# Kernel optimization log

Hardware: AMD Instinct MI355X
Metric: run time of the kernel (lower is better)

The kernel has to match this reference:

```python
import jax, jax.numpy as jnp
import numpy as np

B, N, DIM = 2, 2048, 1024
HEADS, DIM_HEAD = 16, 64
SOFTCAP = 50.0
ROPE_THETA = 10000.0


def setup_inputs() -> dict:
    key = jax.random.key(0)
    k1, k2, k3 = jax.random.split(key, 3)
    x = jax.random.normal(k1, (B, N, DIM), jnp.float32)
    # structured modality positions: (type, offset, length), non-overlapping, in-bounds
    mods = np.zeros((B, 4, 3), np.int64)
    base_offsets = [200, 700, 1200, 1700]
    for b in range(B):
        for m, o in enumerate(base_offsets):
            mods[b, m] = (0, o + b * 16, 256)
    modalities = jnp.asarray(mods)
    gamma = jnp.zeros((DIM,), jnp.float32)           # RMSNorm gamma (init zeros, used as gamma+1)
    w_qkv = jax.random.normal(k2, (DIM, 3 * HEADS * DIM_HEAD), jnp.float32) * 0.02
    w_out = jax.random.normal(k3, (HEADS * DIM_HEAD, DIM), jnp.float32) * 0.02
    return {"x": x, "modalities": modalities, "gamma": gamma, "w_qkv": w_qkv, "w_out": w_out}


def _rotate_half(x):
    # interleaved-pair rotation, matching rotary-embedding-torch default
    x1, x2 = x[..., 0::2], x[..., 1::2]
    return jnp.stack((-x2, x1), axis=-1).reshape(x.shape)


def reference(x, modalities, gamma, w_qkv, w_out):
    b, n, d = x.shape
    h, dh = HEADS, DIM_HEAD
    seq = jnp.arange(n)
    off = modalities[..., 1]      # [b, m]
    length = modalities[..., 2]   # [b, m]

    # --- modality-aware rotary positions (span interior shrunk by offset [1, -1]) ---
    in_span = (seq[None, None, :] >= (off + 1)[:, :, None]) & (seq[None, None, :] < (off + length)[:, :, None])
    is_any_modality = in_span.any(axis=1)                                   # [b, n]
    pos = (seq[None, :] - jnp.cumsum(is_any_modality.astype(jnp.int32), axis=-1)).astype(jnp.float32)

    # --- RMSNorm: l2norm(x) * sqrt(d) * (gamma + 1) ---
    norm = jnp.maximum(jnp.sqrt(jnp.sum(x * x, axis=-1, keepdims=True)), 1e-12)
    xn = x / norm * jnp.sqrt(jnp.float32(d)) * (gamma + 1.0)

    # --- qkv projection, split heads -> [b, h, n, dh] ---
    qkv = (xn @ w_qkv).reshape(b, n, 3, h, dh)
    q, k, v = jnp.moveaxis(qkv, 2, 0)        # each [b, n, h, dh]
    q = jnp.transpose(q, (0, 2, 1, 3))
    k = jnp.transpose(k, (0, 2, 1, 3))
    v = jnp.transpose(v, (0, 2, 1, 3))

    # --- rotary embedding with modality-aware positions ---
    inv_freq = ROPE_THETA ** (-jnp.arange(0, dh, 2, dtype=jnp.float32) / dh)  # [dh/2]
    ang = pos[:, None, :, None] * inv_freq                                    # [b, 1, n, dh/2]
    ang = jnp.repeat(ang, 2, axis=-1)                                         # [b, 1, n, dh]
    cos, sin = jnp.cos(ang), jnp.sin(ang)
    q = q * cos + _rotate_half(q) * sin
    k = k * cos + _rotate_half(k) * sin

    # --- transfusion attention mask: causal OR per-modality bidirectional span ---
    causal_mask = seq[:, None] >= seq[None, :]                                 # [n, n]
    q_ge = seq[None, None, :] >= off[:, :, None]                               # [b, m, n]
    kv_lt = seq[None, None, :] < (off + length)[:, :, None]                    # [b, m, n]
    mod_mask = (q_ge[:, :, :, None] & kv_lt[:, :, None, :]).any(axis=1)        # [b, n, n]
    mask = causal_mask[None] | mod_mask                                        # [b, n, n]

    # --- attention with softclamp(50) ---
    scale = dh ** -0.5
    sim = jnp.einsum('bhid,bhjd->bhij', q, k) * scale
    sim = jnp.tanh(sim / SOFTCAP) * SOFTCAP
    sim = jnp.where(mask[:, None], sim, jnp.finfo(sim.dtype).min)
    attn = jax.nn.softmax(sim, axis=-1)
    out = jnp.einsum('bhij,bhjd->bhid', attn, v)                               # [b, h, n, dh]
    out = jnp.transpose(out, (0, 2, 1, 3)).reshape(b, n, h * dh)
    return out @ w_out
```

## Files before the change

### kernel.cpp

```cpp
#include <hip/hip_runtime.h>
#include <hip/hip_bf16.h>
#include <stdint.h>

#define B_ 2
#define N_ 2048
#define H_ 16
#define DIM_ 1024
#define NH3 3072
#define ROWS (B_*N_)
#define BHN (B_*H_*N_)

typedef __attribute__((ext_vector_type(8))) short bf16x8;
typedef __attribute__((ext_vector_type(4))) float f32x4;
typedef unsigned short u16;

__device__ __forceinline__ u16 f2bf(float f){
  union { float f; uint32_t u; } v; v.f = f;
  return (u16)((v.u + 0x7fffu + ((v.u >> 16) & 1u)) >> 16);
}

#if __has_builtin(__builtin_amdgcn_exp2f)
#define EXP2F(x) __builtin_amdgcn_exp2f(x)
#else
#define EXP2F(x) __expf((x) * 0.6931471805599453f)
#endif
#if __has_builtin(__builtin_amdgcn_rcpf)
#define RCPF(x) __builtin_amdgcn_rcpf(x)
#else
#define RCPF(x) (1.0f / (x))
#endif

#define GLL16(g, l) __builtin_amdgcn_global_load_lds( \
    (const __attribute__((address_space(1))) void*)(g), \
    (__attribute__((address_space(3))) void*)(l), 16, 0, 0)

__global__ __launch_bounds__(256) void k_prep(
    const float* __restrict__ x, const float* __restrict__ gamma,
    const float* __restrict__ wqkv, const float* __restrict__ wout,
    const int* __restrict__ mods,
    u16* __restrict__ xn, u16* __restrict__ wqkvT, u16* __restrict__ woutT,
    float* __restrict__ cosT, float* __restrict__ sinT)
{
  __shared__ float tile[32][33];
  const int bx = blockIdx.x;
  const int tid = threadIdx.x;
  if (bx < 4096){
    const int row = bx;
    const float4 xv = ((const float4*)(x + (size_t)row*DIM_))[tid];
    float ss = xv.x*xv.x + xv.y*xv.y + xv.z*xv.z + xv.w*xv.w;
#pragma unroll
    for (int d = 1; d < 64; d <<= 1) ss += __shfl_xor(ss, d);
    if ((tid & 63) == 0) tile[1][tid >> 6] = ss;
    __syncthreads();
    float tot = tile[1][0] + tile[1][1] + tile[1][2] + tile[1][3];
    float scl = 32.0f / fmaxf(sqrtf(tot), 1e-12f);
    const float4 gv = ((const float4*)gamma)[tid];
    ushort4 o;
    o.x = f2bf(xv.x * scl * (gv.x + 1.0f));
    o.y = f2bf(xv.y * scl * (gv.y + 1.0f));
    o.z = f2bf(xv.z * scl * (gv.z + 1.0f));
    o.w = f2bf(xv.w * scl * (gv.w + 1.0f));
    ((ushort4*)(xn + (size_t)row*DIM_))[tid] = o;
  } else if (bx < 8192){
    const int t = bx - 4096;
    const int bxx = t & 127, by = t >> 7;
    const float* src; u16* dst; int C, bc;
    if (bxx < 96){ src = wqkv; dst = wqkvT; C = NH3;  bc = bxx*32; }
    else         { src = wout; dst = woutT; C = DIM_; bc = (bxx-96)*32; }
    const int R = DIM_;
    const int tx = tid & 31, ty = tid >> 5;
    const int br = by * 32;
#pragma unroll
    for (int i = 0; i < 32; i += 8)
      tile[ty + i][tx] = src[(size_t)(br + ty + i)*C + bc + tx];
    __syncthreads();
#pragma unroll
    for (int i = 0; i < 32; i += 8)
      dst[(size_t)(bc + ty + i)*R + br + tx] = f2bf(tile[tx][ty + i]);
  } else {
    const int t = (bx - 8192)*256 + tid;
    const int f = t & 31, bn = t >> 5;
    const int b = bn >> 11, n = bn & (N_-1);
    int cum = 0;
#pragma unroll
    for (int m = 0; m < 4; ++m){
      const int off = mods[(b*4 + m)*3 + 1];
      const int len = mods[(b*4 + m)*3 + 2];
      cum += min(max(n - off, 0), len - 1);
    }
    const float pos = (float)(n - cum);
    const float inv = powf(10000.0f, -(float)(2*f) / 64.0f);
    float s, c;
    sincosf(pos * inv, &s, &c);
    cosT[t] = c; sinT[t] = s;
  }
}

template<int MODE, int BM>
__global__ __launch_bounds__(256) void k_gemm(
    const u16* __restrict__ A, const u16* __restrict__ Bt,
    int K, int Nc,
    float* __restrict__ outf,
    const float* __restrict__ cosT, const float* __restrict__ sinT,
    u16* __restrict__ qo, u16* __restrict__ ko, u16* __restrict__ vt)
{
  constexpr int MR = BM/32;
  constexpr int RA = BM/8;
  constexpr int CNT = (RA + 16)/4;
  __shared__ u16 lA[BM*64];
  __shared__ u16 lB[128*64];
  const int tid = threadIdx.x;
  const int wid = tid >> 6, lane = tid & 63;
  const int nx = gridDim.x;
  const int orig = blockIdx.y * nx + blockIdx.x;
  const int qq = (nx * gridDim.y) >> 3;
  const int wgid = (orig & 7) * qq + (orig >> 3);
  const int m0 = (wgid % nx) * BM, n0 = (wgid / nx) * 128;
  const int wm = wid >> 1, wn = wid & 1;
  const int srow = lane >> 3, sch = lane & 7;
  const int r16 = lane & 15, g4 = lane >> 4;
  f32x4 acc[MR][4] = {};
  const int ksteps = K >> 6;
  for (int kt = 0; kt < ksteps; ++kt){
    const int kb = kt*64;
    const int gch = sch ^ srow;
#pragma unroll
    for (int i = 0; i < CNT; ++i){
      const int reg = wid*CNT + i;
      if (reg < RA){
        const int row = reg*8 + srow;
        GLL16(A + (size_t)(m0 + row)*K + kb + gch*8, &lA[reg*512]);
      } else {
        const int r2 = reg - RA;
        const int row = r2*8 + srow;
        GLL16(Bt + (size_t)(n0 + row)*K + kb + gch*8, &lB[r2*512]);
      }
    }
    __syncthreads();
#pragma unroll
    for (int t = 0; t < 2; ++t){
      bf16x8 af[MR], bfr[4];
#pragma unroll
      for (int m = 0; m < MR; ++m){
        int row = wm*(BM/2) + m*16 + r16;
        int ch = (t*4 + g4) ^ (r16 & 7);
        af[m] = *(const bf16x8*)&lA[row*64 + ch*8];
      }
#pragma unroll
      for (int n = 0; n < 4; ++n){
        int row = wn*64 + n*16 + r16;
        int ch = (t*4 + g4) ^ (r16 & 7);
        bfr[n] = *(const bf16x8*)&lB[row*64 + ch*8];
      }
#pragma unroll
      for (int m = 0; m < MR; ++m)
#pragma unroll
        for (int n = 0; n < 4; ++n)
          acc[m][n] = __builtin_amdgcn_mfma_f32_16x16x32_bf16(af[m], bfr[n], acc[m][n], 0, 0, 0);
    }
    __syncthreads();
  }
#pragma unroll
  for (int m = 0; m < MR; ++m){
#pragma unroll
    for (int n = 0; n < 4; ++n){
      if constexpr (MODE == 0){
        const int gcol = n0 + wn*64 + n*16 + r16;
        const int s3 = gcol >> 10, hh = (gcol >> 6) & 15, d = gcol & 63;
        const int grow0 = m0 + wm*(BM/2) + m*16 + g4*4;
        const int b = grow0 >> 11, nn0 = grow0 & (N_-1);
        const size_t hb = (size_t)(b*H_ + hh);
        if (s3 == 2){
          uint32_t w01, w23;
          asm("v_cvt_pk_bf16_f32 %0, %1, %2" : "=v"(w01) : "v"(acc[m][n][0]), "v"(acc[m][n][1]));
          asm("v_cvt_pk_bf16_f32 %0, %1, %2" : "=v"(w23) : "v"(acc[m][n][2]), "v"(acc[m][n][3]));
          *reinterpret_cast<uint2*>(&vt[(hb*64 + d)*N_ + nn0]) = make_uint2(w01, w23);
        } else {
#pragma unroll
          for (int r = 0; r < 4; ++r){
            const float v = acc[m][n][r];
            const float part = __shfl_xor(v, 1);
            const int nn = nn0 + r;
            const int pidx = (b*N_ + nn)*32 + (d >> 1);
            const float c = cosT[pidx], sn = sinT[pidx];
            const float rot = (d & 1) ? (v*c + part*sn) : (v*c - part*sn);
            const u16 val = f2bf(rot);
            if (s3 == 0) qo[(hb*N_ + nn)*64 + d] = val;
            else         ko[(hb*N_ + nn)*64 + d] = val;
          }
        }
      } else {
#pragma unroll
        for (int r = 0; r < 4; ++r){
          const int grow = m0 + wm*(BM/2) + m*16 + g4*4 + r;
          const int gcol = n0 + wn*64 + n*16 + r16;
          outf[(size_t)grow*Nc + gcol] = acc[m][n][r];
        }
      }
    }
  }
}

#define PST 68
__global__ __launch_bounds__(512) void k_attn(
    const u16* __restrict__ qb, const u16* __restrict__ kb, const u16* __restrict__ vt,
    const int* __restrict__ mods, u16* __restrict__ xo)
{
  __shared__ u16 lK[64*64];
  __shared__ u16 lV[64*64];
  __shared__ u16 lP[8*16*PST];
  const int tid = threadIdx.x, wid = tid >> 6, lane = tid & 63;
  const int id = blockIdx.x;
  const int xcd = id & 7, rank = id >> 3;
  const int bh = xcd + 8*(rank & 3);
  const int tp = 15 - (rank >> 2);
  const int b = bh >> 4, h = bh & 15;
  const int r16 = lane & 15, g4 = lane >> 4;
  const int srow = lane >> 3, sch = lane & 7;
  int moff[4], mend[4];
#pragma unroll
  for (int m = 0; m < 4; ++m){
    moff[m] = mods[(b*4+m)*3+1];
    mend[m] = moff[m] + mods[(b*4+m)*3+2];
  }
  const u16* kbase = kb + (size_t)bh*N_*64;
  const u16* vbase = vt + (size_t)bh*64*N_;
  u16* lPw = &lP[wid*16*PST];

  const int q0 = tp*128 + wid*16;
  const int i  = q0 + r16;
  const int imax = tp*128 + 127;
  int jmax = 0, jmax0 = 0;
#pragma unroll
  for (int m = 0; m < 4; ++m){
    if (i  >= moff[m]) jmax  = max(jmax,  mend[m]);
    if (q0 >= moff[m]) jmax0 = max(jmax0, mend[m]);
  }
  const int thrmin = max(q0, jmax0 - 1);
  const u16* qrow = qb + ((size_t)bh*N_ + q0 + r16)*64;
  const bf16x8 aq0 = *(const bf16x8*)&qrow[g4*8];
  const bf16x8 aq1 = *(const bf16x8*)&qrow[32 + g4*8];
  f32x4 o[4] = {};
  f32x4 acc_s = {};
  bf16x8 ones;
#pragma unroll
  for (int j = 0; j < 8; ++j) ones[j] = (short)0x3F80;

  const float D1 = 0.18033688011112043f;
  const float D3 = -3.7570183356483704e-07f;

  for (int kt = 0; kt < N_/64; ++kt){
    bool proc = (kt*64 <= imax);
    if (!proc){
#pragma unroll
      for (int m = 0; m < 4; ++m)
        if (imax >= moff[m] && kt*64 < mend[m]) proc = true;
    }
    if (!proc) continue;
    __syncthreads();
    {
      const int gch = sch ^ srow;
      GLL16(kbase + (size_t)(kt*64 + wid*8 + srow)*64 + gch*8, &lK[wid*512]);
      GLL16(vbase + (size_t)(wid*8 + srow)*N_ + kt*64 + gch*8, &lV[wid*512]);
    }
    __syncthreads();
    f32x4 s[4] = {};
    __builtin_amdgcn_s_setprio(1);
#pragma unroll
    for (int cb = 0; cb < 4; ++cb){
#pragma unroll
      for (int t = 0; t < 2; ++t){
        int row = cb*16 + r16;
        int ch = (t*4 + g4) ^ (row & 7);
        bf16x8 bk = *(const bf16x8*)&lK[row*64 + ch*8];
        s[cb] = __builtin_amdgcn_mfma_f32_16x16x32_bf16(bk, t ? aq1 : aq0, s[cb], 0, 0, 0);
      }
    }
    __builtin_amdgcn_s_setprio(0);
    const int thr = max(i, jmax - 1) - kt*64;
    const bool nomask = (kt*64 + 63 <= thrmin);
#pragma unroll
    for (int cb = 0; cb < 4; ++cb){
      float p[4];
#pragma unroll
      for (int r = 0; r < 4; ++r){
        const float sv = s[cb][r];
        const float w = sv*sv;
        p[r] = EXP2F(sv * fmaf(w, D3, D1));
      }
      if (!nomask){
#pragma unroll
        for (int r = 0; r < 4; ++r)
          p[r] = (cb*16 + g4*4 + r <= thr) ? p[r] : 0.0f;
      }
      uint32_t w01, w23;
      asm("v_cvt_pk_bf16_f32 %0, %1, %2" : "=v"(w01) : "v"(p[0]), "v"(p[1]));
      asm("v_cvt_pk_bf16_f32 %0, %1, %2" : "=v"(w23) : "v"(p[2]), "v"(p[3]));
      *reinterpret_cast<uint2*>(&lPw[r16*PST + cb*16 + g4*4]) = make_uint2(w01, w23);
    }
    asm volatile("s_waitcnt lgkmcnt(0)" ::: "memory");
    __builtin_amdgcn_sched_barrier(0);
    union { uint2 h[2]; bf16x8 v; } u0, u1;
    u0.h[0] = *(const uint2*)&lPw[r16*PST + g4*8];
    u0.h[1] = *(const uint2*)&lPw[r16*PST + g4*8 + 4];
    u1.h[0] = *(const uint2*)&lPw[r16*PST + 32 + g4*8];
    u1.h[1] = *(const uint2*)&lPw[r16*PST + 32 + g4*8 + 4];
    __builtin_amdgcn_s_setprio(1);
    acc_s = __builtin_amdgcn_mfma_f32_16x16x32_bf16(u0.v, ones, acc_s, 0, 0, 0);
    acc_s = __builtin_amdgcn_mfma_f32_16x16x32_bf16(u1.v, ones, acc_s, 0, 0, 0);
#pragma unroll
    for (int cb = 0; cb < 4; ++cb){
#pragma unroll
      for (int t = 0; t < 2; ++t){
        int d = cb*16 + r16;
        int ch = (t*4 + g4) ^ (d & 7);
        bf16x8 bv = *(const bf16x8*)&lV[d*64 + ch*8];
        o[cb] = __builtin_amdgcn_mfma_f32_16x16x32_bf16(t ? u1.v : u0.v, bv, o[cb], 0, 0, 0);
      }
    }
    __builtin_amdgcn_s_setprio(0);
  }
#pragma unroll
  for (int r = 0; r < 4; ++r){
    const float linv = RCPF(acc_s[r]);
    const int iq = q0 + g4*4 + r;
#pragma unroll
    for (int cb = 0; cb < 4; ++cb)
      xo[(size_t)(b*N_ + iq)*DIM_ + h*64 + cb*16 + r16] = f2bf(o[cb][r]*linv);
  }
}

extern "C" void kernel_launch(void* const* d_in, const int* in_sizes, int n_in,
                              void* d_out, int out_size, void* d_ws, size_t ws_size,
                              hipStream_t stream){
  const float* x     = (const float*)d_in[0];
  const int*   mods  = (const int*)d_in[1];
  const float* gamma = (const float*)d_in[2];
  const float* wqkv  = (const float*)d_in[3];
  const float* wout  = (const float*)d_in[4];
  float* outp = (float*)d_out;

  char* p = (char*)d_ws;
  auto alloc = [&](size_t bytes) -> char* {
    char* r = p; p += (bytes + 255) & ~(size_t)255; return r;
  };
  float* cosT  = (float*)alloc((size_t)B_*N_*32*4);
  float* sinT  = (float*)alloc((size_t)B_*N_*32*4);
  u16* wqkvT   = (u16*)alloc((size_t)NH3*DIM_*2);
  u16* woutT   = (u16*)alloc((size_t)DIM_*DIM_*2);
  u16* xn      = (u16*)alloc((size_t)ROWS*DIM_*2);
  u16* qbb     = (u16*)alloc((size_t)BHN*64*2);
  u16* kbb     = (u16*)alloc((size_t)BHN*64*2);
  u16* vtb     = (u16*)alloc((size_t)BHN*64*2);
  u16* xo      = (u16*)alloc((size_t)ROWS*DIM_*2);

  k_prep<<<8704, 256, 0, stream>>>(x, gamma, wqkv, wout, mods, xn, wqkvT, woutT, cosT, sinT);
  k_gemm<0,128><<<dim3(ROWS/128, NH3/128), 256, 0, stream>>>(xn, wqkvT, DIM_, NH3, nullptr, cosT, sinT, qbb, kbb, vtb);
  k_attn<<<512, 512, 0, stream>>>(qbb, kbb, vtb, mods, xo);
  k_gemm<1,64><<<dim3(ROWS/64, DIM_/128), 256, 0, stream>>>(xo, woutT, DIM_, DIM_, outp, nullptr, nullptr, nullptr, nullptr, nullptr);
}
```

Measured before the change: 115.9 us.

## Double-buffer K/V LDS tiles in attention to prefetch the next tile

The attention kernel now keeps two LDS buffers each for the K and V tiles. It issues the global-to-LDS load for the next tile that needs processing before computing on the current one, so that global memory latency overlaps with MFMA and softmax work. It also looks ahead to skip fully masked tiles and drops one barrier per iteration. In exchange, LDS use per block grows by 16 KB, and correctness depends on the async loads being complete by the end-of-iteration barrier.

```diff
diff --git a/kernel.cpp b/kernel.cpp
--- a/kernel.cpp
+++ b/kernel.cpp
@@ -206,8 +206,8 @@
     const u16* __restrict__ qb, const u16* __restrict__ kb, const u16* __restrict__ vt,
     const int* __restrict__ mods, u16* __restrict__ xo)
 {
-  __shared__ u16 lK[64*64];
-  __shared__ u16 lV[64*64];
+  __shared__ u16 lK[2][64*64];
+  __shared__ u16 lV[2][64*64];
   __shared__ u16 lP[8*16*PST];
   const int tid = threadIdx.x, wid = tid >> 6, lane = tid & 63;
   const int id = blockIdx.x;
@@ -249,21 +249,31 @@
   const float D1 = 0.18033688011112043f;
   const float D3 = -3.7570183356483704e-07f;
 
-  for (int kt = 0; kt < N_/64; ++kt){
-    bool proc = (kt*64 <= imax);
-    if (!proc){
-#pragma unroll
-      for (int m = 0; m < 4; ++m)
-        if (imax >= moff[m] && kt*64 < mend[m]) proc = true;
-    }
-    if (!proc) continue;
-    __syncthreads();
-    {
-      const int gch = sch ^ srow;
-      GLL16(kbase + (size_t)(kt*64 + wid*8 + srow)*64 + gch*8, &lK[wid*512]);
-      GLL16(vbase + (size_t)(wid*8 + srow)*N_ + kt*64 + gch*8, &lV[wid*512]);
-    }
-    __syncthreads();
+  auto proc = [&](int kt)->bool{
+    if (kt*64 <= imax) return true;
+    bool p = false;
+#pragma unroll
+    for (int m = 0; m < 4; ++m)
+      if (imax >= moff[m] && kt*64 < mend[m]) p = true;
+    return p;
+  };
+  auto stage = [&](int kt, int bi){
+    const int gch = sch ^ srow;
+    GLL16(kbase + (size_t)(kt*64 + wid*8 + srow)*64 + gch*8, &lK[bi][wid*512]);
+    GLL16(vbase + (size_t)(wid*8 + srow)*N_ + kt*64 + gch*8, &lV[bi][wid*512]);
+  };
+
+  int kt = 0;
+  int nkt = 1;
+  while (nkt < 32 && !proc(nkt)) ++nkt;
+  stage(0, 0);
+  __syncthreads();
+  int cur = 0;
+
+  while (true){
+    if (nkt < 32) stage(nkt, cur ^ 1);
+    const u16* lKc = lK[cur];
+    const u16* lVc = lV[cur];
     f32x4 s[4] = {};
     __builtin_amdgcn_s_setprio(1);
 #pragma unroll
@@ -272,7 +282,7 @@
       for (int t = 0; t < 2; ++t){
         int row = cb*16 + r16;
         int ch = (t*4 + g4) ^ (row & 7);
-        bf16x8 bk = *(const bf16x8*)&lK[row*64 + ch*8];
+        bf16x8 bk = *(const bf16x8*)&lKc[row*64 + ch*8];
         s[cb] = __builtin_amdgcn_mfma_f32_16x16x32_bf16(bk, t ? aq1 : aq0, s[cb], 0, 0, 0);
       }
     }
@@ -314,11 +324,17 @@
       for (int t = 0; t < 2; ++t){
         int d = cb*16 + r16;
         int ch = (t*4 + g4) ^ (d & 7);
-        bf16x8 bv = *(const bf16x8*)&lV[d*64 + ch*8];
+        bf16x8 bv = *(const bf16x8*)&lVc[d*64 + ch*8];
         o[cb] = __builtin_amdgcn_mfma_f32_16x16x32_bf16(t ? u1.v : u0.v, bv, o[cb], 0, 0, 0);
       }
     }
     __builtin_amdgcn_s_setprio(0);
+    if (nkt >= 32) break;
+    __syncthreads();
+    cur ^= 1;
+    kt = nkt;
+    ++nkt;
+    while (nkt < 32 && !proc(nkt)) ++nkt;
   }
 #pragma unroll
   for (int r = 0; r < 4; ++r){
```

Result: no change. 116.3 us (+0.4%).
